# Kernel optimization log

Hardware: AMD Instinct MI355X
Metric: run time of the kernel (lower is better)

Reference implementation:

```python
import jax, jax.numpy as jnp
import numpy as np

EPS = 1e-5
NPOINT = 1024
NSAMPLE = 32


def _bn(x, gamma, beta, axes):
    # batch-norm in training mode (biased variance), channel-last
    m = jnp.mean(x, axes, keepdims=True)
    v = jnp.var(x, axes, keepdims=True)
    return (x - m) * jax.lax.rsqrt(v + EPS) * gamma + beta


def _fps(xyz, npoint):
    # xyz: [B, N, 3] -> indices [B, npoint]; deterministic start at index 0
    xyz = jax.lax.stop_gradient(xyz)
    B, N, _ = xyz.shape

    def step(carry, _):
        dist, far = carry
        c = jnp.take_along_axis(xyz, far[:, None, None], axis=1)  # [B,1,3]
        d = jnp.sum((xyz - c) ** 2, -1)                            # [B,N]
        dist = jnp.minimum(dist, d)
        return (dist, jnp.argmax(dist, -1).astype(jnp.int32)), far

    init = (jnp.full((B, N), 1e10, xyz.dtype), jnp.zeros((B,), jnp.int32))
    _, idx = jax.lax.scan(step, init, None, length=npoint)
    return idx.T  # [B, npoint]


def _sqdist(src, dst):
    # [B,S,C],[B,N,C] -> [B,S,N]
    d = -2.0 * jnp.einsum('bsc,bnc->bsn', src, dst)
    d += jnp.sum(src ** 2, -1)[:, :, None]
    d += jnp.sum(dst ** 2, -1)[:, None, :]
    return d


def _gather(p, idx):
    # p: [B,N,C], idx: [B,...] -> [B,...,C]
    return jax.vmap(lambda a, i: a[i])(p, idx)


def setup_inputs() -> dict:
    key = jax.random.key(0)
    ks = jax.random.split(key, 12)
    B, N, D = 8, 4096, 64
    inp = {
        'xyz': jax.random.normal(ks[0], (B, 3, N), jnp.float32),
        'points': jax.random.normal(ks[1], (B, D, N), jnp.float32),
        # mlp convs (1x1 Conv2d == per-point linear): [out,in]
        'c1_w': jax.random.normal(ks[2], (64, 64), jnp.float32) / 8.0,
        'c1_b': jnp.zeros((64,), jnp.float32),
        'g1': jnp.ones((64,), jnp.float32), 'b1': jnp.zeros((64,), jnp.float32),
        'c2_w': jax.random.normal(ks[3], (128, 64), jnp.float32) / 8.0,
        'c2_b': jnp.zeros((128,), jnp.float32),
        'g2': jnp.ones((128,), jnp.float32), 'b2': jnp.zeros((128,), jnp.float32),
        # weightnet: 3 -> 8 -> 8 -> 16
        'w0_w': jax.random.normal(ks[4], (8, 3), jnp.float32) / np.sqrt(3.0),
        'w0_b': jnp.zeros((8,), jnp.float32),
        'w0_g': jnp.ones((8,), jnp.float32), 'w0_be': jnp.zeros((8,), jnp.float32),
        'w1_w': jax.random.normal(ks[5], (8, 8), jnp.float32) / np.sqrt(8.0),
        'w1_b': jnp.zeros((8,), jnp.float32),
        'w1_g': jnp.ones((8,), jnp.float32), 'w1_be': jnp.zeros((8,), jnp.float32),
        'w2_w': jax.random.normal(ks[6], (16, 8), jnp.float32) / np.sqrt(8.0),
        'w2_b': jnp.zeros((16,), jnp.float32),
        'w2_g': jnp.ones((16,), jnp.float32), 'w2_be': jnp.zeros((16,), jnp.float32),
        # final linear: 16*128 -> 128
        'lin_w': jax.random.normal(ks[7], (128, 16 * 128), jnp.float32) / np.sqrt(2048.0),
        'lin_b': jnp.zeros((128,), jnp.float32),
        'lg': jnp.ones((128,), jnp.float32), 'lb': jnp.zeros((128,), jnp.float32),
    }
    return inp


def reference(xyz, points, c1_w, c1_b, g1, b1, c2_w, c2_b, g2, b2,
              w0_w, w0_b, w0_g, w0_be, w1_w, w1_b, w1_g, w1_be,
              w2_w, w2_b, w2_g, w2_be, lin_w, lin_b, lg, lb):
    B = xyz.shape[0]
    X = jnp.transpose(xyz, (0, 2, 1))      # [B,N,3]
    P = jnp.transpose(points, (0, 2, 1))   # [B,N,D]

    fps_idx = _fps(X, NPOINT)                                      # [B,S]
    new_xyz = jnp.take_along_axis(X, fps_idx[:, :, None], axis=1)  # [B,S,3]

    sqr = _sqdist(jax.lax.stop_gradient(new_xyz), jax.lax.stop_gradient(X))
    _, nidx = jax.lax.top_k(-sqr, NSAMPLE)                         # [B,S,K]

    neigh_xyz = _gather(X, nidx)                                   # [B,S,K,3]
    off = neigh_xyz - new_xyz[:, :, None, :]                       # [B,S,K,3]
    f = _gather(P, nidx)                                           # [B,S,K,D]

    # per-point MLP (1x1 convs + BN2d over (B,K,S) + relu)
    for W, bias, g, be in ((c1_w, c1_b, g1, b1), (c2_w, c2_b, g2, b2)):
        f = jax.nn.relu(_bn(jnp.einsum('bskd,cd->bskc', f, W) + bias, g, be, (0, 1, 2)))

    # WeightNet on offsets
    w = off
    for W, bias, g, be in ((w0_w, w0_b, w0_g, w0_be),
                           (w1_w, w1_b, w1_g, w1_be),
                           (w2_w, w2_b, w2_g, w2_be)):
        w = jax.nn.relu(_bn(jnp.einsum('bskd,cd->bskc', w, W) + bias, g, be, (0, 1, 2)))

    # weighted aggregation over neighbors: [B,S,Cl,16] -> [B,S,Cl*16]
    feats = jnp.einsum('bskc,bskw->bscw', f, w).reshape(B, NPOINT, -1)
    y = feats @ lin_w.T + lin_b                                    # [B,S,128]
    y = jax.nn.relu(_bn(y, lg, lb, (0, 1)))

    return jnp.transpose(new_xyz, (0, 2, 1)), jnp.transpose(y, (0, 2, 1))
```

## Files before the change

kernel.cpp:

```cpp
#include <hip/hip_runtime.h>
#include <hip/hip_bf16.h>

#define BB 8
#define NN 4096
#define DD 64
#define SS 1024
#define KK 32
#define C1 64
#define C2 128

typedef unsigned int uint32;
typedef unsigned long long uint64;

constexpr int BSK = BB * SS * KK;
constexpr int BS  = BB * SS;

#define ST_S1_C1 0
#define ST_S2_C1 64
#define ST_S1_C2 128
#define ST_S2_C2 256
#define ST_S1_W0 384
#define ST_S2_W0 392
#define ST_S1_W1 400
#define ST_S2_W1 408
// ... 634 lines not shown
                                                 const float* __restrict__ w2_b,
                                                 const float* __restrict__ params,
                                                 int blk, int t, float* wg) {
    for (int idx = t; idx < KK * 16; idx += 256) {
        int k = idx >> 4, cw = idx & 15;
        size_t oo = ((size_t)blk * KK + k) * 3;
        float o0 = offs[oo], o1 = offs[oo + 1], o2 = offs[oo + 2];
        float h0[8], h1[8];
#pragma unroll
        for (int j = 0; j < 8; j++) {
            float hh = w0_b[j];
            hh = fmaf(o0, w0_w[j * 3 + 0], hh);
            hh = fmaf(o1, w0_w[j * 3 + 1], hh);
            hh = fmaf(o2, w0_w[j * 3 + 2], hh);
            h0[j] = fmaxf(fmaf(hh, params[PA_A_W0 + j], params[PA_C_W0 + j]), 0.f);
        }
#pragma unroll
        for (int j = 0; j < 8; j++) {
            float hh = w1_b[j];
#pragma unroll
            for (int q = 0; q < 8; q++) hh = fmaf(h0[q], w1_w[j * 8 + q], hh);
            h1[j] = fmaxf(fmaf(hh, params[PA_A_W1 + j], params[PA_C_W1 + j]), 0.f);
        }
        float h = w2_b[cw];
#pragma unroll
        for (int q = 0; q < 8; q++) h = fmaf(h1[q], w2_w[cw * 8 + q], h);
        wg[idx] = fmaxf(fmaf(h, params[PA_A_W2 + cw], params[PA_C_W2 + cw]), 0.f);
    }
}

__global__ __launch_bounds__(256) void tail_nl2(const float* __restrict__ f2pre,
                                                const float* __restrict__ offs,
                                                const float* __restrict__ w0_w,
                                                const float* __restrict__ w0_b,
                                                const float* __restrict__ w1_w,
                                                const float* __restrict__ w1_b,
                                                const float* __restrict__ w2_w,
                                                const float* __restrict__ w2_b,
                                                const float* __restrict__ params,
                                                float* __restrict__ featsF) {
    __shared__ __align__(16) float sm[6656];
    float* f2    = sm;
    float* wg    = sm + 4096;
    float* feats = sm + 4608;
    int blk = blockIdx.x, t = threadIdx.x;
    weightnet_to_lds(offs, w0_w, w0_b, w1_w, w1_b, w2_w, w2_b, params, blk, t, wg);
    {
        int c = t & 127;
        float a2 = params[PA_A_C2 + c], cc2 = params[PA_C_C2 + c];
#pragma unroll
        for (int i = 0; i < 16; i++) {
            float v = f2pre[(size_t)blk * 4096 + i * 256 + t];
            f2[i * 256 + t] = fmaxf(fmaf(v, a2, cc2), 0.f);
        }
    }
    __syncthreads();
    {
        int cc = t & 127, wh = t >> 7;
        float acc[8];
#pragma unroll
        for (int i = 0; i < 8; i++) acc[i] = 0.f;
        for (int k = 0; k < KK; k++) {
            float fv = f2[k * 128 + cc];
            const float4 wa = *(const float4*)&wg[k * 16 + 8 * wh];
            const float4 wb = *(const float4*)&wg[k * 16 + 8 * wh + 4];
            acc[0] = fmaf(fv, wa.x, acc[0]);
            acc[1] = fmaf(fv, wa.y, acc[1]);
            acc[2] = fmaf(fv, wa.z, acc[2]);
            acc[3] = fmaf(fv, wa.w, acc[3]);
            acc[4] = fmaf(fv, wb.x, acc[4]);
            acc[5] = fmaf(fv, wb.y, acc[5]);
            acc[6] = fmaf(fv, wb.z, acc[6]);
            acc[7] = fmaf(fv, wb.w, acc[7]);
        }
        *(float4*)&feats[cc * 16 + 8 * wh]     = *(float4*)&acc[0];
        *(float4*)&feats[cc * 16 + 8 * wh + 4] = *(float4*)&acc[4];
    }
    __syncthreads();
#pragma unroll
    for (int i = 0; i < 8; i++)
        featsF[(size_t)blk * 2048 + i * 256 + t] = feats[i * 256 + t];
}

__global__ __launch_bounds__(256) void fused_tail_nl(
        const __hip_bfloat16* __restrict__ ptsT, const int* __restrict__ nidx,
        const float* __restrict__ offs,
        const float* __restrict__ w1t, const float* __restrict__ c1_b,
        const float* __restrict__ w2t, const float* __restrict__ c2_b,
        const float* __restrict__ w0_w, const float* __restrict__ w0_b,
        const float* __restrict__ w1_w, const float* __restrict__ w1_b,
        const float* __restrict__ w2_w, const float* __restrict__ w2_b,
        const float* __restrict__ params, float* __restrict__ featsF) {
    __shared__ __align__(16) float sm[8704];
    float* pts   = sm;
    float* f1    = sm + 2048;
    float* f2    = sm + 4096;
    float* wg    = sm + 8192;
    int blk = blockIdx.x, t = threadIdx.x;
    int b = blk >> 10;
    stage_pts(ptsT, nidx, blk, b, t, pts);
    weightnet_to_lds(offs, w0_w, w0_b, w1_w, w1_b, w2_w, w2_b, params, blk, t, wg);
    __syncthreads();
    {
        int c = t & 63, kg = t >> 6;
        float a1 = params[PA_A_C1 + c], cc1 = params[PA_C_C1 + c], bias = c1_b[c];
        float acc[8];
#pragma unroll
        for (int j = 0; j < 8; j++) acc[j] = bias;
        for (int d4 = 0; d4 < 16; d4++) {
            float w0 = w1t[(4 * d4 + 0) * 64 + c];
            float w1v = w1t[(4 * d4 + 1) * 64 + c];
            float w2v = w1t[(4 * d4 + 2) * 64 + c];
            float w3 = w1t[(4 * d4 + 3) * 64 + c];
#pragma unroll
            for (int j = 0; j < 8; j++) {
                const float4 p = *(const float4*)&pts[(kg + 4 * j) * 64 + 4 * d4];
                acc[j] = fmaf(p.x, w0, acc[j]);
                acc[j] = fmaf(p.y, w1v, acc[j]);
                acc[j] = fmaf(p.z, w2v, acc[j]);
                acc[j] = fmaf(p.w, w3, acc[j]);
            }
        }
#pragma unroll
        for (int j = 0; j < 8; j++)
            f1[(kg + 4 * j) * 64 + c] = fmaxf(fmaf(acc[j], a1, cc1), 0.f);
    }
    __syncthreads();
    {
        int c = t & 127, kg = t >> 7;
        float a2 = params[PA_A_C2 + c], cc2 = params[PA_C_C2 + c], bias = c2_b[c];
        float acc[16];
#pragma unroll
        for (int j = 0; j < 16; j++) acc[j] = bias;
        for (int d4 = 0; d4 < 16; d4++) {
            float w0 = w2t[(4 * d4 + 0) * 128 + c];
            float w1v = w2t[(4 * d4 + 1) * 128 + c];
            float w2v = w2t[(4 * d4 + 2) * 128 + c];
            float w3 = w2t[(4 * d4 + 3) * 128 + c];
#pragma unroll
            for (int j = 0; j < 16; j++) {
                const float4 p = *(const float4*)&f1[(kg + 2 * j) * 64 + 4 * d4];
                acc[j] = fmaf(p.x, w0, acc[j]);
                acc[j] = fmaf(p.y, w1v, acc[j]);
                acc[j] = fmaf(p.z, w2v, acc[j]);
                acc[j] = fmaf(p.w, w3, acc[j]);
            }
        }
#pragma unroll
        for (int j = 0; j < 16; j++)
            f2[(kg + 2 * j) * 128 + c] = fmaxf(fmaf(acc[j], a2, cc2), 0.f);
    }
    __syncthreads();
    {
        int cc = t & 127, wh = t >> 7;
        float acc[8];
#pragma unroll
        for (int i = 0; i < 8; i++) acc[i] = 0.f;
        for (int k = 0; k < KK; k++) {
            float fv = f2[k * 128 + cc];
            const float4 wa = *(const float4*)&wg[k * 16 + 8 * wh];
            const float4 wb = *(const float4*)&wg[k * 16 + 8 * wh + 4];
            acc[0] = fmaf(fv, wa.x, acc[0]);
            acc[1] = fmaf(fv, wa.y, acc[1]);
            acc[2] = fmaf(fv, wa.z, acc[2]);
            acc[3] = fmaf(fv, wa.w, acc[3]);
            acc[4] = fmaf(fv, wb.x, acc[4]);
            acc[5] = fmaf(fv, wb.y, acc[5]);
            acc[6] = fmaf(fv, wb.z, acc[6]);
            acc[7] = fmaf(fv, wb.w, acc[7]);
        }
        *(float4*)&pts[cc * 16 + 8 * wh]     = *(float4*)&acc[0];
        *(float4*)&pts[cc * 16 + 8 * wh + 4] = *(float4*)&acc[4];
    }
    __syncthreads();
#pragma unroll
    for (int i = 0; i < 8; i++)
        featsF[(size_t)blk * 2048 + i * 256 + t] = sm[i * 256 + t];
}

__global__ __launch_bounds__(256) void fused_tail(
        const __hip_bfloat16* __restrict__ ptsT, const int* __restrict__ nidx,
        const float* __restrict__ offs,
        const float* __restrict__ w1t, const float* __restrict__ c1_b,
        const float* __restrict__ w2t, const float* __restrict__ c2_b,
        const float* __restrict__ w0_w, const float* __restrict__ w0_b,
        const float* __restrict__ w1_w, const float* __restrict__ w1_b,
        const float* __restrict__ w2_w, const float* __restrict__ w2_b,
        const __hip_bfloat16* __restrict__ linB, const float* __restrict__ lin_b,
        const float* __restrict__ params, float* __restrict__ stats,
        float* __restrict__ ypre) {
    __shared__ __align__(16) float sm[8704];
    float* pts   = sm;
    float* f1    = sm + 2048;
    float* f2    = sm + 4096;
    float* wg    = sm + 8192;
    int blk = blockIdx.x, t = threadIdx.x;
    int b = blk >> 10;
    int slot = blk & (N_SLOTS - 1);
    stage_pts(ptsT, nidx, blk, b, t, pts);
    weightnet_to_lds(offs, w0_w, w0_b, w1_w, w1_b, w2_w, w2_b, params, blk, t, wg);
    __syncthreads();
    {
        int c = t & 63, kg = t >> 6;
        float a1 = params[PA_A_C1 + c], cc1 = params[PA_C_C1 + c], bias = c1_b[c];
        float acc[8];
#pragma unroll
        for (int j = 0; j < 8; j++) acc[j] = bias;
        for (int d4 = 0; d4 < 16; d4++) {
            float w0 = w1t[(4 * d4 + 0) * 64 + c];
            float w1v = w1t[(4 * d4 + 1) * 64 + c];
            float w2v = w1t[(4 * d4 + 2) * 64 + c];
            float w3 = w1t[(4 * d4 + 3) * 64 + c];
#pragma unroll
            for (int j = 0; j < 8; j++) {
                const float4 p = *(const float4*)&pts[(kg + 4 * j) * 64 + 4 * d4];
                acc[j] = fmaf(p.x, w0, acc[j]);
                acc[j] = fmaf(p.y, w1v, acc[j]);
                acc[j] = fmaf(p.z, w2v, acc[j]);
                acc[j] = fmaf(p.w, w3, acc[j]);
            }
        }
#pragma unroll
        for (int j = 0; j < 8; j++)
            f1[(kg + 4 * j) * 64 + c] = fmaxf(fmaf(acc[j], a1, cc1), 0.f);
    }
    __syncthreads();
    {
        int c = t & 127, kg = t >> 7;
        float a2 = params[PA_A_C2 + c], cc2 = params[PA_C_C2 + c], bias = c2_b[c];
        float acc[16];
#pragma unroll
        for (int j = 0; j < 16; j++) acc[j] = bias;
        for (int d4 = 0; d4 < 16; d4++) {
            float w0 = w2t[(4 * d4 + 0) * 128 + c];
            float w1v = w2t[(4 * d4 + 1) * 128 + c];
            float w2v = w2t[(4 * d4 + 2) * 128 + c];
            float w3 = w2t[(4 * d4 + 3) * 128 + c];
#pragma unroll
            for (int j = 0; j < 16; j++) {
                const float4 p = *(const float4*)&f1[(kg + 2 * j) * 64 + 4 * d4];
                acc[j] = fmaf(p.x, w0, acc[j]);
                acc[j] = fmaf(p.y, w1v, acc[j]);
                acc[j] = fmaf(p.z, w2v, acc[j]);
                acc[j] = fmaf(p.w, w3, acc[j]);
            }
        }
#pragma unroll
        for (int j = 0; j < 16; j++)
            f2[(kg + 2 * j) * 128 + c] = fmaxf(fmaf(acc[j], a2, cc2), 0.f);
    }
    __syncthreads();
    {
        int cc = t & 127, wh = t >> 7;
        float acc[8];
#pragma unroll
        for (int i = 0; i < 8; i++) acc[i] = 0.f;
        for (int k = 0; k < KK; k++) {
            float fv = f2[k * 128 + cc];
            const float4 wa = *(const float4*)&wg[k * 16 + 8 * wh];
            const float4 wb = *(const float4*)&wg[k * 16 + 8 * wh + 4];
            acc[0] = fmaf(fv, wa.x, acc[0]);
            acc[1] = fmaf(fv, wa.y, acc[1]);
            acc[2] = fmaf(fv, wa.z, acc[2]);
            acc[3] = fmaf(fv, wa.w, acc[3]);
            acc[4] = fmaf(fv, wb.x, acc[4]);
            acc[5] = fmaf(fv, wb.y, acc[5]);
            acc[6] = fmaf(fv, wb.z, acc[6]);
            acc[7] = fmaf(fv, wb.w, acc[7]);
        }
        *(float4*)&pts[cc * 16 + 8 * wh]     = *(float4*)&acc[0];
        *(float4*)&pts[cc * 16 + 8 * wh + 4] = *(float4*)&acc[4];
    }
    __syncthreads();
    float* feats = pts;
    {
        int wv = t >> 6, lane = t & 63;
        float4 fv[8];
#pragma unroll
        for (int j0 = 0; j0 < 8; j0++)
            fv[j0] = *(const float4*)&feats[(j0 * 64 + lane) * 4];
        for (int oi = 0; oi < 32; oi++) {
            int o = wv * 32 + oi;
            const uint2* lw = (const uint2*)(linB + (size_t)o * 2048);
            float acc = 0.f;
#pragma unroll
            for (int j0 = 0; j0 < 8; j0++) {
                uint2 u = lw[j0 * 64 + lane];
                acc = fmaf(fv[j0].x, __uint_as_float(u.x << 16), acc);
                acc = fmaf(fv[j0].y, __uint_as_float(u.x & 0xffff0000u), acc);
                acc = fmaf(fv[j0].z, __uint_as_float(u.y << 16), acc);
                acc = fmaf(fv[j0].w, __uint_as_float(u.y & 0xffff0000u), acc);
            }
            acc = wave_sum_f32(acc);
            if (lane == LIN_WRITER) {
                float y = acc + lin_b[o];
                ypre[(size_t)blk * 128 + o] = y;
                atomicAdd(&stats[slot * ST_STRIDE + ST_S1_Y + o], y);
                atomicAdd(&stats[slot * ST_STRIDE + ST_S2_Y + o], y * y);
            }
        }
    }
}

__global__ __launch_bounds__(256) void linear_mm(const float* __restrict__ featsF,
                                                 const __hip_bfloat16* __restrict__ linB,
                                                 const float* __restrict__ lin_b,
                                                 float* __restrict__ stats,
                                                 float* __restrict__ ypre) {
    __shared__ __align__(16) unsigned short Ah[32 * 72];
    __shared__ __align__(16) unsigned short Al[32 * 72];
    __shared__ __align__(16) unsigned short Bsm[128 * 72];
    int t = threadIdx.x;
    int q0 = blockIdx.x * 32;
    int slot = blockIdx.x & (N_SLOTS - 1);
    int qa = t >> 3, pa = t & 7;
    int ob = t >> 1, pb = t & 1;
    int lane = t & 63, wid = t >> 6;
    int wr = wid >> 1, wc = wid & 1;
    int lg = lane >> 4, ln = lane & 15;
    int am = wr * 16 + ln;
    int qb_base = q0 + wr * 16 + lg * 4;

    f32x4v acc0 = {0.f, 0.f, 0.f, 0.f};
    f32x4v acc1 = {0.f, 0.f, 0.f, 0.f};
    f32x4v acc2 = {0.f, 0.f, 0.f, 0.f};
    f32x4v acc3 = {0.f, 0.f, 0.f, 0.f};

    const uint4* gA0 = (const uint4*)(featsF + (size_t)(q0 + qa) * 2048 + pa * 8);
    const uint4* gB0 = (const uint4*)(linB + (size_t)ob * 2048 + pb * 32);

    uint4 ra0, ra1, rb0, rb1, rb2, rb3;
    ra0 = gA0[0]; ra1 = gA0[1];
    rb0 = gB0[0]; rb1 = gB0[1]; rb2 = gB0[2]; rb3 = gB0[3];

    for (int kc = 0; kc < 32; kc++) {
        __syncthreads();
        {
            float f0 = __uint_as_float(ra0.x), f1v = __uint_as_float(ra0.y);
            float f2v = __uint_as_float(ra0.z), f3 = __uint_as_float(ra0.w);
            float f4v = __uint_as_float(ra1.x), f5 = __uint_as_float(ra1.y);
            float f6 = __uint_as_float(ra1.z), f7 = __uint_as_float(ra1.w);
            uint32 h0 = bf16rne(f0), h1 = bf16rne(f1v), h2 = bf16rne(f2v), h3 = bf16rne(f3);
            uint32 h4 = bf16rne(f4v), h5 = bf16rne(f5), h6 = bf16rne(f6), h7 = bf16rne(f7);
            uint4 hv;
            hv.x = h0 | (h1 << 16); hv.y = h2 | (h3 << 16);
            hv.z = h4 | (h5 << 16); hv.w = h6 | (h7 << 16);
            *(uint4*)&Ah[qa * 72 + pa * 8] = hv;
            uint32 l0 = bf16rne(f0 - __uint_as_float(h0 << 16));
            uint32 l1 = bf16rne(f1v - __uint_as_float(h1 << 16));
            uint32 l2 = bf16rne(f2v - __uint_as_float(h2 << 16));
            uint32 l3 = bf16rne(f3 - __uint_as_float(h3 << 16));
            uint32 l4 = bf16rne(f4v - __uint_as_float(h4 << 16));
            uint32 l5 = bf16rne(f5 - __uint_as_float(h5 << 16));
            uint32 l6 = bf16rne(f6 - __uint_as_float(h6 << 16));
            uint32 l7 = bf16rne(f7 - __uint_as_float(h7 << 16));
            uint4 lv;
            lv.x = l0 | (l1 << 16); lv.y = l2 | (l3 << 16);
            lv.z = l4 | (l5 << 16); lv.w = l6 | (l7 << 16);
            *(uint4*)&Al[qa * 72 + pa * 8] = lv;
            *(uint4*)&Bsm[ob * 72 + pb * 32 + 0]  = rb0;
            *(uint4*)&Bsm[ob * 72 + pb * 32 + 8]  = rb1;
            *(uint4*)&Bsm[ob * 72 + pb * 32 + 16] = rb2;
            *(uint4*)&Bsm[ob * 72 + pb * 32 + 24] = rb3;
        }
        __syncthreads();
        if (kc + 1 < 32) {
            const uint4* gA = gA0 + (kc + 1) * 16;
            const uint4* gB = gB0 + (kc + 1) * 8;
            ra0 = gA[0]; ra1 = gA[1];
            rb0 = gB[0]; rb1 = gB[1]; rb2 = gB[2]; rb3 = gB[3];
        }
#pragma unroll
        for (int s = 0; s < 2; s++) {
            int ko = s * 32 + lg * 8;
            bf16x8 ah = *(const bf16x8*)&Ah[am * 72 + ko];
            bf16x8 al = *(const bf16x8*)&Al[am * 72 + ko];
            bf16x8 b0 = *(const bf16x8*)&Bsm[(wc * 64 + 0  + ln) * 72 + ko];
            bf16x8 b1 = *(const bf16x8*)&Bsm[(wc * 64 + 16 + ln) * 72 + ko];
            bf16x8 b2 = *(const bf16x8*)&Bsm[(wc * 64 + 32 + ln) * 72 + ko];
            bf16x8 b3 = *(const bf16x8*)&Bsm[(wc * 64 + 48 + ln) * 72 + ko];
            acc0 = __builtin_amdgcn_mfma_f32_16x16x32_bf16(ah, b0, acc0, 0, 0, 0);
            acc0 = __builtin_amdgcn_mfma_f32_16x16x32_bf16(al, b0, acc0, 0, 0, 0);
            acc1 = __builtin_amdgcn_mfma_f32_16x16x32_bf16(ah, b1, acc1, 0, 0, 0);
            acc1 = __builtin_amdgcn_mfma_f32_16x16x32_bf16(al, b1, acc1, 0, 0, 0);
            acc2 = __builtin_amdgcn_mfma_f32_16x16x32_bf16(ah, b2, acc2, 0, 0, 0);
            acc2 = __builtin_amdgcn_mfma_f32_16x16x32_bf16(al, b2, acc2, 0, 0, 0);
            acc3 = __builtin_amdgcn_mfma_f32_16x16x32_bf16(ah, b3, acc3, 0, 0, 0);
            acc3 = __builtin_amdgcn_mfma_f32_16x16x32_bf16(al, b3, acc3, 0, 0, 0);
        }
    }
    {
        int o0 = wc * 64 + 0  + ln;
        int o1 = wc * 64 + 16 + ln;
        int o2 = wc * 64 + 32 + ln;
        int o3 = wc * 64 + 48 + ln;
        float lb0 = lin_b[o0], lb1 = lin_b[o1], lb2 = lin_b[o2], lb3 = lin_b[o3];
        float s1a = 0.f, s2a = 0.f, s1b = 0.f, s2b = 0.f;
        float s1c = 0.f, s2c = 0.f, s1d = 0.f, s2d = 0.f;
#pragma unroll
        for (int r = 0; r < 4; r++) {
            size_t qrow = (size_t)(qb_base + r) * 128;
            float y0 = acc0[r] + lb0;
            float y1 = acc1[r] + lb1;
            float y2 = acc2[r] + lb2;
            float y3 = acc3[r] + lb3;
            ypre[qrow + o0] = y0;
            ypre[qrow + o1] = y1;
            ypre[qrow + o2] = y2;
            ypre[qrow + o3] = y3;
            s1a += y0; s2a += y0 * y0;
            s1b += y1; s2b += y1 * y1;
            s1c += y2; s2c += y2 * y2;
            s1d += y3; s2d += y3 * y3;
        }
        atomicAdd(&stats[slot * ST_STRIDE + ST_S1_Y + o0], s1a);
        atomicAdd(&stats[slot * ST_STRIDE + ST_S2_Y + o0], s2a);
        atomicAdd(&stats[slot * ST_STRIDE + ST_S1_Y + o1], s1b);
        atomicAdd(&stats[slot * ST_STRIDE + ST_S2_Y + o1], s2b);
        atomicAdd(&stats[slot * ST_STRIDE + ST_S1_Y + o2], s1c);
        atomicAdd(&stats[slot * ST_STRIDE + ST_S2_Y + o2], s2c);
        atomicAdd(&stats[slot * ST_STRIDE + ST_S1_Y + o3], s1d);
        atomicAdd(&stats[slot * ST_STRIDE + ST_S2_Y + o3], s2d);
    }
}

__global__ __launch_bounds__(256) void bn_y(const float* __restrict__ ypre,
                                            const float* __restrict__ stats,
                                            const float* __restrict__ lg,
                                            const float* __restrict__ lb,
                                            float* __restrict__ out1) {
    __shared__ float tile[64 * 133];
    __shared__ float pa[128], pc[128];
    int blk = blockIdx.x;
    int b = blk >> 4;
    int s0 = (blk & 15) * 64;
    int t = threadIdx.x;
    if (t < 128) {
        float s1 = 0.f, s2 = 0.f;
        for (int s = 0; s < N_SLOTS; s++) {
            s1 += stats[s * ST_STRIDE + ST_S1_Y + t];
            s2 += stats[s * ST_STRIDE + ST_S2_Y + t];
        }
        const float inv = 1.f / (float)BS;
        float m = s1 * inv;
        float v = s2 * inv - m * m;
        float a = lg[t] * rsqrtf(v + 1e-5f);
        pa[t] = a;
        pc[t] = lb[t] - m * a;
    }
#pragma unroll
    for (int i = 0; i < 32; i++) {
        int idx = i * 256 + t;
        int s = idx >> 7, c = idx & 127;
        tile[s * 133 + c] = ypre[(((size_t)b << 10) + s0 + s) * 128 + c];
    }
    __syncthreads();
#pragma unroll
    for (int i = 0; i < 32; i++) {
        int idx = i * 256 + t;
        int c = idx >> 6, s = idx & 63;
        float v = tile[s * 133 + c];
        out1[((size_t)b * 128 + c) * 1024 + s0 + s] =
            fmaxf(fmaf(v, pa[c], pc[c]), 0.f);
    }
}

extern "C" void kernel_launch(void* const* d_in, const int* in_sizes, int n_in,
                              void* d_out, int out_size, void* d_ws, size_t ws_size,
                              hipStream_t stream) {
    const float* xyz    = (const float*)d_in[0];
    const float* points = (const float*)d_in[1];
    const float* c1_w = (const float*)d_in[2];
    const float* c1_b = (const float*)d_in[3];
    const float* g1   = (const float*)d_in[4];
    const float* b1   = (const float*)d_in[5];
    const float* c2_w = (const float*)d_in[6];
    const float* c2_b = (const float*)d_in[7];
    const float* g2   = (const float*)d_in[8];
    const float* b2   = (const float*)d_in[9];
    const float* w0_w = (const float*)d_in[10];
    const float* w0_b = (const float*)d_in[11];
    const float* w0_g = (const float*)d_in[12];
    const float* w0_be= (const float*)d_in[13];
    const float* w1_w = (const float*)d_in[14];
    const float* w1_b = (const float*)d_in[15];
    const float* w1_g = (const float*)d_in[16];
    const float* w1_be= (const float*)d_in[17];
    const float* w2_w = (const float*)d_in[18];
    const float* w2_b = (const float*)d_in[19];
    const float* w2_g = (const float*)d_in[20];
    const float* w2_be= (const float*)d_in[21];
    const float* lin_w= (const float*)d_in[22];
    const float* lin_b= (const float*)d_in[23];
    const float* lg   = (const float*)d_in[24];
    const float* lb   = (const float*)d_in[25];

    float* out0 = (float*)d_out;
    float* out1 = out0 + (size_t)BB * 3 * SS;

    char* wsb = (char*)d_ws;
    int*   nidx    = (int*)(wsb + 0);
    float* offs    = (float*)(wsb + 1048576);
    float* new_xyz = (float*)(wsb + 4194304);
    float* ypre    = (float*)(wsb + 4292608);
    __hip_bfloat16* ptsT = (__hip_bfloat16*)(wsb + 8486912);
    float* w1t     = (float*)(wsb + 12681216);
    float* w2t     = (float*)(wsb + 12697600);
    __hip_bfloat16* linB = (__hip_bfloat16*)(wsb + 12730368);
    float* stats   = (float*)(wsb + 13254656);
    float* params  = (float*)(wsb + 13434880);
    float* featsF  = (float*)(wsb + 13437696);
    float* f1pre   = featsF;
    float* f2pre   = (float*)(wsb + 80546560);

    const size_t NEED1 = 13437696ull + 67108864ull;
    const size_t NEED2 = 80546560ull + 134217728ull;
    const int tier = (ws_size >= NEED2) ? 2 : (ws_size >= NEED1) ? 1 : 0;

    hipMemsetAsync(stats, 0, N_SLOTS * ST_STRIDE * sizeof(float), stream);

    prep_fps<<<1592, 256, 0, stream>>>(points, ptsT, c1_w, c2_w, lin_w, w1t, w2t,
                                       linB, xyz, new_xyz, out0);
    knn_wave<<<BS / 4, 256, 0, stream>>>(xyz, new_xyz, nidx, offs);

    pass_a<<<BS, 256, 0, stream>>>(ptsT, nidx, offs, w1t, c1_b, w0_w, w0_b, stats,
                                   f1pre, tier == 2 ? 1 : 0);
    finalize_two<<<2, 128, 0, stream>>>(stats, params,
                                        g1, b1, ST_S1_C1, ST_S2_C1, PA_A_C1, PA_C_C1, 64, 1.f / BSK,
                                        w0_g, w0_be, ST_S1_W0, ST_S2_W0, PA_A_W0, PA_C_W0, 8, 1.f / BSK);

    if (tier == 2) {
        pass_b2<<<BS, 256, 0, stream>>>(f1pre, offs, w2t, c2_b,
                                        w0_w, w0_b, w1_w, w1_b, params, stats, f2pre);
    } else {
        pass_b<<<BS, 256, 0, stream>>>(ptsT, nidx, offs, w1t, c1_b, w2t, c2_b,
                                       w0_w, w0_b, w1_w, w1_b, params, stats);
    }
    finalize_two<<<2, 128, 0, stream>>>(stats, params,
                                        g2, b2, ST_S1_C2, ST_S2_C2, PA_A_C2, PA_C_C2, 128, 1.f / BSK,
                                        w1_g, w1_be, ST_S1_W1, ST_S2_W1, PA_A_W1, PA_C_W1, 8, 1.f / BSK);

    pass_w2<<<BSK / 256, 256, 0, stream>>>(offs, w0_w, w0_b, w1_w, w1_b, w2_w, w2_b,
                                           params, stats);
    finalize_bn<<<1, 128, 0, stream>>>(stats, params, w2_g, w2_be,
                                       ST_S1_W2, ST_S2_W2, PA_A_W2, PA_C_W2, 16, 1.f / BSK);

    if (tier == 2) {
        tail_nl2<<<BS, 256, 0, stream>>>(f2pre, offs, w0_w, w0_b, w1_w, w1_b,
                                         w2_w, w2_b, params, featsF);
        linear_mm<<<BS / 32, 256, 0, stream>>>(featsF, linB, lin_b, stats, ypre);
    } else if (tier == 1) {
        fused_tail_nl<<<BS, 256, 0, stream>>>(ptsT, nidx, offs, w1t, c1_b, w2t, c2_b,
                                              w0_w, w0_b, w1_w, w1_b, w2_w, w2_b,
                                              params, featsF);
        linear_mm<<<BS / 32, 256, 0, stream>>>(featsF, linB, lin_b, stats, ypre);
    } else {
        fused_tail<<<BS, 256, 0, stream>>>(ptsT, nidx, offs, w1t, c1_b, w2t, c2_b,
                                           w0_w, w0_b, w1_w, w1_b, w2_w, w2_b,
                                           linB, lin_b, params, stats, ypre);
    }

    bn_y<<<BB * 16, 256, 0, stream>>>(ypre, stats, lg, lb, out1);
}
```

Measured before the change: 1.117 ms.

## Halve linear GEMM row tile and double-buffer shared memory in linear_mm

```diff
diff --git a/kernel.cpp b/kernel.cpp
--- a/kernel.cpp
+++ b/kernel.cpp
@@ -960,125 +960,97 @@
     }
 }
 
-__global__ __launch_bounds__(256) void linear_mm(const float* __restrict__ featsF,
-                                                 const __hip_bfloat16* __restrict__ linB,
-                                                 const float* __restrict__ lin_b,
-                                                 float* __restrict__ stats,
-                                                 float* __restrict__ ypre) {
-    __shared__ __align__(16) unsigned short Ah[32 * 72];
-    __shared__ __align__(16) unsigned short Al[32 * 72];
-    __shared__ __align__(16) unsigned short Bsm[128 * 72];
+__global__ __launch_bounds__(256) void linear_mm16(const float* __restrict__ featsF,
+                                                   const __hip_bfloat16* __restrict__ linB,
+                                                   const float* __restrict__ lin_b,
+                                                   float* __restrict__ stats,
+                                                   float* __restrict__ ypre) {
+    __shared__ __align__(16) unsigned short Ah[2][16 * 72];
+    __shared__ __align__(16) unsigned short Al[2][16 * 72];
+    __shared__ __align__(16) unsigned short Bsm[2][128 * 72];
     int t = threadIdx.x;
-    int q0 = blockIdx.x * 32;
+    int q0 = blockIdx.x * 16;
     int slot = blockIdx.x & (N_SLOTS - 1);
-    int qa = t >> 3, pa = t & 7;
+    int qa = t >> 4, pa = t & 15;
     int ob = t >> 1, pb = t & 1;
-    int lane = t & 63, wid = t >> 6;
-    int wr = wid >> 1, wc = wid & 1;
+    int lane = t & 63, w = t >> 6;
     int lg = lane >> 4, ln = lane & 15;
-    int am = wr * 16 + ln;
-    int qb_base = q0 + wr * 16 + lg * 4;
+    int qb_base = q0 + lg * 4;
 
     f32x4v acc0 = {0.f, 0.f, 0.f, 0.f};
     f32x4v acc1 = {0.f, 0.f, 0.f, 0.f};
-    f32x4v acc2 = {0.f, 0.f, 0.f, 0.f};
-    f32x4v acc3 = {0.f, 0.f, 0.f, 0.f};
-
-    const uint4* gA0 = (const uint4*)(featsF + (size_t)(q0 + qa) * 2048 + pa * 8);
-    const uint4* gB0 = (const uint4*)(linB + (size_t)ob * 2048 + pb * 32);
-
-    uint4 ra0, ra1, rb0, rb1, rb2, rb3;
-    ra0 = gA0[0]; ra1 = gA0[1];
-    rb0 = gB0[0]; rb1 = gB0[1]; rb2 = gB0[2]; rb3 = gB0[3];
+
+    const uint4* gA0 = (const uint4*)(featsF + (size_t)(q0 + qa) * 2048);
+    const uint4* gB0 = (const uint4*)(linB + (size_t)ob * 2048);
+
+    uint4 ra, rb0, rb1, rb2, rb3;
+    ra  = gA0[pa];
+    rb0 = gB0[pb * 4 + 0];
+    rb1 = gB0[pb * 4 + 1];
+    rb2 = gB0[pb * 4 + 2];
+    rb3 = gB0[pb * 4 + 3];
 
     for (int kc = 0; kc < 32; kc++) {
-        __syncthreads();
+        int buf = kc & 1;
         {
-            float f0 = __uint_as_float(ra0.x), f1v = __uint_as_float(ra0.y);
-            float f2v = __uint_as_float(ra0.z), f3 = __uint_as_float(ra0.w);
-            float f4v = __uint_as_float(ra1.x), f5 = __uint_as_float(ra1.y);
-            float f6 = __uint_as_float(ra1.z), f7 = __uint_as_float(ra1.w);
+            float f0 = __uint_as_float(ra.x), f1v = __uint_as_float(ra.y);
+            float f2v = __uint_as_float(ra.z), f3 = __uint_as_float(ra.w);
             uint32 h0 = bf16rne(f0), h1 = bf16rne(f1v), h2 = bf16rne(f2v), h3 = bf16rne(f3);
-            uint32 h4 = bf16rne(f4v), h5 = bf16rne(f5), h6 = bf16rne(f6), h7 = bf16rne(f7);
-            uint4 hv;
+            uint2 hv;
             hv.x = h0 | (h1 << 16); hv.y = h2 | (h3 << 16);
-            hv.z = h4 | (h5 << 16); hv.w = h6 | (h7 << 16);
-            *(uint4*)&Ah[qa * 72 + pa * 8] = hv;
+            *(uint2*)&Ah[buf][qa * 72 + pa * 4] = hv;
             uint32 l0 = bf16rne(f0 - __uint_as_float(h0 << 16));
             uint32 l1 = bf16rne(f1v - __uint_as_float(h1 << 16));
             uint32 l2 = bf16rne(f2v - __uint_as_float(h2 << 16));
             uint32 l3 = bf16rne(f3 - __uint_as_float(h3 << 16));
-            uint32 l4 = bf16rne(f4v - __uint_as_float(h4 << 16));
-            uint32 l5 = bf16rne(f5 - __uint_as_float(h5 << 16));
-            uint32 l6 = bf16rne(f6 - __uint_as_float(h6 << 16));
-            uint32 l7 = bf16rne(f7 - __uint_as_float(h7 << 16));
-            uint4 lv;
+            uint2 lv;
             lv.x = l0 | (l1 << 16); lv.y = l2 | (l3 << 16);
-            lv.z = l4 | (l5 << 16); lv.w = l6 | (l7 << 16);
-            *(uint4*)&Al[qa * 72 + pa * 8] = lv;
-            *(uint4*)&Bsm[ob * 72 + pb * 32 + 0]  = rb0;
-            *(uint4*)&Bsm[ob * 72 + pb * 32 + 8]  = rb1;
-            *(uint4*)&Bsm[ob * 72 + pb * 32 + 16] = rb2;
-            *(uint4*)&Bsm[ob * 72 + pb * 32 + 24] = rb3;
+            *(uint2*)&Al[buf][qa * 72 + pa * 4] = lv;
+            *(uint4*)&Bsm[buf][ob * 72 + pb * 32 + 0]  = rb0;
+            *(uint4*)&Bsm[buf][ob * 72 + pb * 32 + 8]  = rb1;
+            *(uint4*)&Bsm[buf][ob * 72 + pb * 32 + 16] = rb2;
+            *(uint4*)&Bsm[buf][ob * 72 + pb * 32 + 24] = rb3;
         }
         __syncthreads();
         if (kc + 1 < 32) {
-            const uint4* gA = gA0 + (kc + 1) * 16;
-            const uint4* gB = gB0 + (kc + 1) * 8;
-            ra0 = gA[0]; ra1 = gA[1];
-            rb0 = gB[0]; rb1 = gB[1]; rb2 = gB[2]; rb3 = gB[3];
+            ra  = gA0[(kc + 1) * 16 + pa];
+            rb0 = gB0[(kc + 1) * 8 + pb * 4 + 0];
+            rb1 = gB0[(kc + 1) * 8 + pb * 4 + 1];
+            rb2 = gB0[(kc + 1) * 8 + pb * 4 + 2];
+            rb3 = gB0[(kc + 1) * 8 + pb * 4 + 3];
         }
 #pragma unroll
         for (int s = 0; s < 2; s++) {
             int ko = s * 32 + lg * 8;
-            bf16x8 ah = *(const bf16x8*)&Ah[am * 72 + ko];
-            bf16x8 al = *(const bf16x8*)&Al[am * 72 + ko];
-            bf16x8 b0 = *(const bf16x8*)&Bsm[(wc * 64 + 0  + ln) * 72 + ko];
-            bf16x8 b1 = *(const bf16x8*)&Bsm[(wc * 64 + 16 + ln) * 72 + ko];
-            bf16x8 b2 = *(const bf16x8*)&Bsm[(wc * 64 + 32 + ln) * 72 + ko];
-            bf16x8 b3 = *(const bf16x8*)&Bsm[(wc * 64 + 48 + ln) * 72 + ko];
+            bf16x8 ah = *(const bf16x8*)&Ah[buf][ln * 72 + ko];
+            bf16x8 al = *(const bf16x8*)&Al[buf][ln * 72 + ko];
+            bf16x8 b0 = *(const bf16x8*)&Bsm[buf][(w * 32 + 0  + ln) * 72 + ko];
+            bf16x8 b1 = *(const bf16x8*)&Bsm[buf][(w * 32 + 16 + ln) * 72 + ko];
             acc0 = __builtin_amdgcn_mfma_f32_16x16x32_bf16(ah, b0, acc0, 0, 0, 0);
             acc0 = __builtin_amdgcn_mfma_f32_16x16x32_bf16(al, b0, acc0, 0, 0, 0);
             acc1 = __builtin_amdgcn_mfma_f32_16x16x32_bf16(ah, b1, acc1, 0, 0, 0);
             acc1 = __builtin_amdgcn_mfma_f32_16x16x32_bf16(al, b1, acc1, 0, 0, 0);
-            acc2 = __builtin_amdgcn_mfma_f32_16x16x32_bf16(ah, b2, acc2, 0, 0, 0);
-            acc2 = __builtin_amdgcn_mfma_f32_16x16x32_bf16(al, b2, acc2, 0, 0, 0);
-            acc3 = __builtin_amdgcn_mfma_f32_16x16x32_bf16(ah, b3, acc3, 0, 0, 0);
-            acc3 = __builtin_amdgcn_mfma_f32_16x16x32_bf16(al, b3, acc3, 0, 0, 0);
-        }
-    }
-    {
-        int o0 = wc * 64 + 0  + ln;
-        int o1 = wc * 64 + 16 + ln;
-        int o2 = wc * 64 + 32 + ln;
-        int o3 = wc * 64 + 48 + ln;
-        float lb0 = lin_b[o0], lb1 = lin_b[o1], lb2 = lin_b[o2], lb3 = lin_b[o3];
+        }
+    }
+    {
+        int o0 = w * 32 + 0  + ln;
+        int o1 = w * 32 + 16 + ln;
+        float lb0 = lin_b[o0], lb1 = lin_b[o1];
         float s1a = 0.f, s2a = 0.f, s1b = 0.f, s2b = 0.f;
-        float s1c = 0.f, s2c = 0.f, s1d = 0.f, s2d = 0.f;
 #pragma unroll
         for (int r = 0; r < 4; r++) {
             size_t qrow = (size_t)(qb_base + r) * 128;
             float y0 = acc0[r] + lb0;
             float y1 = acc1[r] + lb1;
-            float y2 = acc2[r] + lb2;
-            float y3 = acc3[r] + lb3;
             ypre[qrow + o0] = y0;
             ypre[qrow + o1] = y1;
-            ypre[qrow + o2] = y2;
-            ypre[qrow + o3] = y3;
             s1a += y0; s2a += y0 * y0;
             s1b += y1; s2b += y1 * y1;
-            s1c += y2; s2c += y2 * y2;
-            s1d += y3; s2d += y3 * y3;
         }
         atomicAdd(&stats[slot * ST_STRIDE + ST_S1_Y + o0], s1a);
         atomicAdd(&stats[slot * ST_STRIDE + ST_S2_Y + o0], s2a);
         atomicAdd(&stats[slot * ST_STRIDE + ST_S1_Y + o1], s1b);
         atomicAdd(&stats[slot * ST_STRIDE + ST_S2_Y + o1], s2b);
-        atomicAdd(&stats[slot * ST_STRIDE + ST_S1_Y + o2], s1c);
-        atomicAdd(&stats[slot * ST_STRIDE + ST_S2_Y + o2], s2c);
-        atomicAdd(&stats[slot * ST_STRIDE + ST_S1_Y + o3], s1d);
-        atomicAdd(&stats[slot * ST_STRIDE + ST_S2_Y + o3], s2d);
     }
 }
 
@@ -1206,12 +1178,12 @@
     if (tier == 2) {
         tail_nl2<<<BS, 256, 0, stream>>>(f2pre, offs, w0_w, w0_b, w1_w, w1_b,
                                          w2_w, w2_b, params, featsF);
-        linear_mm<<<BS / 32, 256, 0, stream>>>(featsF, linB, lin_b, stats, ypre);
+        linear_mm16<<<BS / 16, 256, 0, stream>>>(featsF, linB, lin_b, stats, ypre);
     } else if (tier == 1) {
         fused_tail_nl<<<BS, 256, 0, stream>>>(ptsT, nidx, offs, w1t, c1_b, w2t, c2_b,
                                               w0_w, w0_b, w1_w, w1_b, w2_w, w2_b,
                                               params, featsF);
-        linear_mm<<<BS / 32, 256, 0, stream>>>(featsF, linB, lin_b, stats, ypre);
+        linear_mm16<<<BS / 16, 256, 0, stream>>>(featsF, linB, lin_b, stats, ypre);
     } else {
         fused_tail<<<BS, 256, 0, stream>>>(ptsT, nidx, offs, w1t, c1_b, w2t, c2_b,
                                            w0_w, w0_b, w1_w, w1_b, w2_w, w2_b,
```

After: 1.113 ms. Within noise of the previous version (-0.4%).
